# Performance work log

Measured on AMD Instinct MI355X. Metric: run time of the kernel, lower is better.

## Reference

```python
import jax, jax.numpy as jnp
import numpy as np

D_MODEL = 768
HEADS = 12
D_K = D_MODEL // HEADS
NEG = -1e9


def setup_inputs() -> dict:
    key = jax.random.key(0)
    ks = jax.random.split(key, 12)
    B, S = 1, 4096
    q = jax.random.normal(ks[0], (B, S, D_MODEL), dtype=jnp.float32)
    k = jax.random.normal(ks[1], (B, S, D_MODEL), dtype=jnp.float32)
    v = jax.random.normal(ks[2], (B, S, D_MODEL), dtype=jnp.float32)
    mask = jax.random.randint(ks[3], (B, S, S), 0, 2, dtype=jnp.int32)
    sc = 1.0 / np.sqrt(D_MODEL)
    Wq = jax.random.normal(ks[4], (D_MODEL, D_MODEL), dtype=jnp.float32) * sc
    Wk = jax.random.normal(ks[5], (D_MODEL, D_MODEL), dtype=jnp.float32) * sc
    Wv = jax.random.normal(ks[6], (D_MODEL, D_MODEL), dtype=jnp.float32) * sc
    Wo = jax.random.normal(ks[7], (D_MODEL, D_MODEL), dtype=jnp.float32) * sc
    bq = jnp.zeros((D_MODEL,), jnp.float32)
    bk = jnp.zeros((D_MODEL,), jnp.float32)
    bv = jnp.zeros((D_MODEL,), jnp.float32)
    bo = jnp.zeros((D_MODEL,), jnp.float32)
    return {"q": q, "k": k, "v": v, "Wq": Wq, "bq": bq, "Wk": Wk, "bk": bk,
            "Wv": Wv, "bv": bv, "Wo": Wo, "bo": bo, "mask": mask}


def reference(q, k, v, Wq, bq, Wk, bk, Wv, bv, Wo, bo, mask) -> jnp.ndarray:
    B, S, _ = q.shape
    # projections (x @ W^T + b, matching nn.Linear)
    qh = (q @ Wq.T + bq).reshape(B, S, HEADS, D_K).transpose(0, 2, 1, 3)  # [B,h,S,dk]
    kh = (k @ Wk.T + bk).reshape(B, S, HEADS, D_K).transpose(0, 2, 1, 3)
    vh = (v @ Wv.T + bv).reshape(B, S, HEADS, D_K).transpose(0, 2, 1, 3)
    scores = jnp.einsum('bhqd,bhkd->bhqk', qh, kh) / jnp.sqrt(jnp.float32(D_K))
    scores = jnp.where(mask[:, None, :, :] == 0, jnp.float32(NEG), scores)
    attn = jax.nn.softmax(scores, axis=-1)  # dropout disabled (eval mode)
    ctx = jnp.einsum('bhqk,bhkd->bhqd', attn, vh)
    concat = ctx.transpose(0, 2, 1, 3).reshape(B, S, D_MODEL)
    return concat @ Wo.T + bo
```

## Files before the change

### kernel.cpp

```cpp
#include <hip/hip_runtime.h>

#define S_LEN 4096
#define DMODEL 768
#define NHEADS 12
#define DKH 64
#define SC2F 0.18033688011112042f

typedef __attribute__((ext_vector_type(8))) short bf16x8;
typedef __attribute__((ext_vector_type(4))) float f32x4;
typedef __attribute__((ext_vector_type(16))) float f32x16;
typedef __attribute__((ext_vector_type(4))) short s16x4;

#define AS1 __attribute__((address_space(1)))
#define AS3 __attribute__((address_space(3)))

__device__ __forceinline__ short f2bf(float f) {
    union { float f; unsigned u; } x; x.f = f;
    unsigned r = x.u + 0x7fffu + ((x.u >> 16) & 1u);
    return (short)(r >> 16);
}

__device__ __forceinline__ float bf2f(short s) {
    union { unsigned u; float f; } x;
    x.u = ((unsigned)(unsigned short)s) << 16;
    return x.f;
}

__device__ __forceinline__ void gload_lds16(const void* g, void* l) {
    __builtin_amdgcn_global_load_lds((const AS1 void*)g, (AS3 void*)l, 16, 0, 0);
}

__global__ void cvt_all(const float* __restrict__ q, const float* __restrict__ k,
                        const float* __restrict__ v, const float* __restrict__ Wq,
                        const float* __restrict__ Wk, const float* __restrict__ Wv,
                        const float* __restrict__ Wo,
                        short* __restrict__ qb, short* __restrict__ kb,
                        short* __restrict__ vb, short* __restrict__ Wb,
                        const int* __restrict__ mask, unsigned long long* __restrict__ mpT) {
    const int z = blockIdx.z;
    if (z >= 7) {
        int lane = threadIdx.x & 63;
        int wid = (blockIdx.x * blockDim.x + threadIdx.x) >> 6;
        int nw = (gridDim.x * blockDim.x) >> 6;
        int base = (z - 7) * 65536;
        for (int w = base + wid; w < base + 65536; w += nw) {
            int m = mask[(size_t)w * 64 + lane];
            unsigned long long b = __ballot(m != 0);
            if (lane == 0) mpT[(size_t)(w & 63) * S_LEN + (w >> 6)] = b;
        }
        return;
    }
    const float* s;
    short* d;
    int n8;
    if (z < 3) {
        s = z == 0 ? q : z == 1 ? k : v;
        d = z == 0 ? qb : z == 1 ? kb : vb;
        n8 = S_LEN * DMODEL / 8;
    } else {
        s = z == 3 ? Wq : z == 4 ? Wk : z == 5 ? Wv : Wo;
        d = Wb + (size_t)(z - 3) * (DMODEL * DMODEL);
        n8 = DMODEL * DMODEL / 8;
    }
    int stride = gridDim.x * blockDim.x;
    for (int i = blockIdx.x * blockDim.x + threadIdx.x; i < n8; i += stride) {
        float4 x = ((const float4*)s)[2 * i];
        float4 y = ((const float4*)s)[2 * i + 1];
        bf16x8 o;
        o[0] = f2bf(x.x); o[1] = f2bf(x.y); o[2] = f2bf(x.z); o[3] = f2bf(x.w);
        o[4] = f2bf(y.x); o[5] = f2bf(y.y); o[6] = f2bf(y.z); o[7] = f2bf(y.w);
        ((bf16x8*)d)[i] = o;
    }
}

__global__ __launch_bounds__(256) void qkv_gemm(
    const short* __restrict__ qA, const short* __restrict__ kA, const short* __restrict__ vA,
    const short* __restrict__ Wqb, const short* __restrict__ Wkb, const short* __restrict__ Wvb,
    const float* __restrict__ bq, const float* __restrict__ bk, const float* __restrict__ bv,
    short* __restrict__ Qh, short* __restrict__ Kh, short* __restrict__ Vt)
{
    const int z = blockIdx.z;
    const short* A = z == 0 ? qA : z == 1 ? kA : vA;
    const short* B = z == 0 ? Wqb : z == 1 ? Wkb : Wvb;
    const float* bias = z == 0 ? bq : z == 1 ? bk : bv;

    __shared__ __align__(16) short As[128 * 64];
    __shared__ __align__(16) short Bs[128 * 64];
    const int tid = threadIdx.x;
    const int wv = tid >> 6, l = tid & 63;
    const int wr = wv >> 1, wc = wv & 1;
    const int g = l >> 4, hl = l & 15;
    const int m0 = blockIdx.x * 128, n0 = blockIdx.y * 128;
    const int Kd = DMODEL;

    f32x4 acc[4][4] = {};

    for (int kt = 0; kt < Kd; kt += 64) {
        __syncthreads();
        #pragma unroll
        for (int i = 0; i < 4; ++i) {
            int row = i * 32 + wv * 8 + (l >> 3);
            int csrc = (l & 7) ^ (row & 7);
            gload_lds16(A + (size_t)(m0 + row) * Kd + kt + csrc * 8, As + (i * 32 + wv * 8) * 64);
        }
        #pragma unroll
        for (int i = 0; i < 4; ++i) {
            int row = i * 32 + wv * 8 + (l >> 3);
            int csrc = (l & 7) ^ (row & 7);
            gload_lds16(B + (size_t)(n0 + row) * Kd + kt + csrc * 8, Bs + (i * 32 + wv * 8) * 64);
        }
        __syncthreads();
        #pragma unroll
        for (int s = 0; s < 2; ++s) {
            bf16x8 af[4], bf[4];
            #pragma unroll
            for (int m = 0; m < 4; ++m) {
                int row = wr * 64 + m * 16 + hl;
                int ch = (s * 4 + g) ^ (row & 7);
                af[m] = *(const bf16x8*)(As + row * 64 + ch * 8);
            }
            #pragma unroll
            for (int n = 0; n < 4; ++n) {
                int row = wc * 64 + n * 16 + hl;
                int ch = (s * 4 + g) ^ (row & 7);
                bf[n] = *(const bf16x8*)(Bs + row * 64 + ch * 8);
            }
            #pragma unroll
            for (int m = 0; m < 4; ++m)
                #pragma unroll
                for (int n = 0; n < 4; ++n)
                    acc[m][n] = __builtin_amdgcn_mfma_f32_16x16x32_bf16(af[m], bf[n], acc[m][n], 0, 0, 0);
        }
    }

    const float scale = (z == 0) ? SC2F : 1.0f;
    #pragma unroll
    for (int m = 0; m < 4; ++m) {
        #pragma unroll
        for (int n = 0; n < 4; ++n) {
            int gsb = m0 + wr * 64 + m * 16 + g * 4;
            int go = n0 + wc * 64 + n * 16 + hl;
            float bvv = bias[go];
            int hh = go >> 6, d = go & 63;
            if (z == 2) {
                s16x4 p;
                #pragma unroll
                for (int r = 0; r < 4; ++r) p[r] = f2bf(acc[m][n][r] + bvv);
                int gsb2 = (gsb & ~12) | ((gsb & 4) << 1) | ((gsb & 8) >> 1);
                *(s16x4*)(Vt + (size_t)hh * DKH * S_LEN + (size_t)d * S_LEN + gsb2) = p;
            } else {
                short* O = z ? Kh : Qh;
                #pragma unroll
                for (int r = 0; r < 4; ++r)
                    O[(size_t)hh * S_LEN * DKH + (size_t)(gsb + r) * DKH + d] = f2bf((acc[m][n][r] + bvv) * scale);
            }
        }
    }
}

__global__ __launch_bounds__(256) void gemm_out(
    const short* __restrict__ po, const float* __restrict__ pd,
    const short* __restrict__ B,
    const float* __restrict__ bias, float* __restrict__ O)
{
    __shared__ __align__(16) short As[128 * 64];
    __shared__ __align__(16) short Bs[128 * 64];
    const int tid = threadIdx.x;
    const int wv = tid >> 6, l = tid & 63;
    const int wr = wv >> 1, wc = wv & 1;
    const int g = l >> 4, hl = l & 15;
    const int m0 = blockIdx.x * 128, n0 = blockIdx.y * 128;
    const int Kd = DMODEL;

    f32x4 acc[4][4] = {};

    for (int kt = 0; kt < Kd; kt += 64) {
        __syncthreads();
        const int h = kt >> 6;
        #pragma unroll
        for (int i = 0; i < 4; ++i) {
            int row = i * 32 + wv * 8 + (l >> 3);
            int csrc = (l & 7) ^ (row & 7);
            size_t base = ((size_t)h * S_LEN + m0 + row) * DKH + csrc * 8;
            bf16x8 a = *(const bf16x8*)(po + base);
            bf16x8 b = *(const bf16x8*)(po + (size_t)NHEADS * S_LEN * DKH + base);
            float inv = 1.0f / (pd[h * S_LEN + m0 + row] + pd[NHEADS * S_LEN + h * S_LEN + m0 + row]);
            bf16x8 o;
            #pragma unroll
            for (int e = 0; e < 8; ++e)
                o[e] = f2bf((bf2f(a[e]) + bf2f(b[e])) * inv);
            *(bf16x8*)(As + (i * 32 + wv * 8) * 64 + l * 8) = o;
        }
        #pragma unroll
        for (int i = 0; i < 4; ++i) {
            int row = i * 32 + wv * 8 + (l >> 3);
            int csrc = (l & 7) ^ (row & 7);
            gload_lds16(B + (size_t)(n0 + row) * Kd + kt + csrc * 8, Bs + (i * 32 + wv * 8) * 64);
        }
        __syncthreads();
        #pragma unroll
        for (int s = 0; s < 2; ++s) {
            bf16x8 af[4], bf[4];
            #pragma unroll
            for (int m = 0; m < 4; ++m) {
                int row = wr * 64 + m * 16 + hl;
                int ch = (s * 4 + g) ^ (row & 7);
                af[m] = *(const bf16x8*)(As + row * 64 + ch * 8);
            }
            #pragma unroll
            for (int n = 0; n < 4; ++n) {
                int row = wc * 64 + n * 16 + hl;
                int ch = (s * 4 + g) ^ (row & 7);
                bf[n] = *(const bf16x8*)(Bs + row * 64 + ch * 8);
            }
            #pragma unroll
            for (int m = 0; m < 4; ++m)
                #pragma unroll
                for (int n = 0; n < 4; ++n)
                    acc[m][n] = __builtin_amdgcn_mfma_f32_16x16x32_bf16(af[m], bf[n], acc[m][n], 0, 0, 0);
        }
    }

    #pragma unroll
    for (int m = 0; m < 4; ++m) {
        #pragma unroll
        for (int n = 0; n < 4; ++n) {
            int gsb = m0 + wr * 64 + m * 16 + g * 4;
            int go = n0 + wc * 64 + n * 16 + hl;
            float bvv = bias[go];
            #pragma unroll
            for (int r = 0; r < 4; ++r)
                O[(size_t)(gsb + r) * DMODEL + go] = acc[m][n][r] + bvv;
        }
    }
}

__global__ __launch_bounds__(512) void flash_attn6(
    const short* __restrict__ Qh, const short* __restrict__ Kh,
    const short* __restrict__ Vt, const unsigned long long* __restrict__ mpT,
    short* __restrict__ po, float* __restrict__ pd)
{
    __shared__ __align__(16) char pool[35328];

    const int tid = threadIdx.x;
    const int wv = tid >> 6, l = tid & 63;
    const int wq = wv >> 1, sp = wv & 1;
    const int hi = l >> 5, q = l & 31;

    int fid = blockIdx.x;
    int g = (fid & 7) * 96 + (fid >> 3);
    const int h = g >> 6;
    const int sub = g & 63;
    const int half = sub >> 5;
    const int q0 = (sub & 31) * 128;

    const short* Khb = Kh + (size_t)h * S_LEN * DKH;
    const short* Vtb = Vt + (size_t)h * DKH * S_LEN;
    const int qrow = q0 + wq * 32 + q;

    bf16x8 aq[4];
    #pragma unroll
    for (int s = 0; s < 4; ++s)
        aq[s] = *(const bf16x8*)(Qh + (size_t)h * S_LEN * DKH + (size_t)qrow * DKH + s * 16 + hi * 8);

    f32x16 acc[2] = {};
    float dacc[4] = {0.f, 0.f, 0.f, 0.f};

    short* Kl = (short*)(pool + sp * 8192);
    short* Vl = (short*)(pool + 16384 + sp * 8192);

    for (int i = 0; i < 16; ++i) {
        const int kt = half * 32 + i * 2 + sp;
        const int kv0 = kt * 64;
        __syncthreads();
        #pragma unroll
        for (int j = 0; j < 2; ++j) {
            int rp = (wq * 2 + j) * 4 + (l >> 4);
            int x = (l & 15) ^ (rp & 15);
            int row = rp * 2 + (x >> 3);
            int c = x & 7;
            gload_lds16(Khb + (size_t)(kv0 + row) * DKH + c * 8, Kl + (wq * 2 + j) * 512);
            gload_lds16(Vtb + (size_t)row * S_LEN + kv0 + c * 8, Vl + (wq * 2 + j) * 512);
        }
        unsigned long long w = mpT[(size_t)kt * S_LEN + qrow];
        __syncthreads();

        unsigned long long w2 = w >> (hi * 4);
        unsigned mlo = (unsigned)w2, mhi2 = (unsigned)(w2 >> 32);

        #pragma unroll
        for (int t = 0; t < 2; ++t) {
            const unsigned msk = t ? mhi2 : mlo;
            f32x16 st = {};
            __builtin_amdgcn_s_setprio(1);
            #pragma unroll
            for (int s = 0; s < 4; ++s) {
                int rowb = t * 32 + q;
                int rp = rowb >> 1;
                int ch = (((rowb & 1) << 3) + (s * 2 + hi)) ^ (rp & 15);
                bf16x8 kf = *(const bf16x8*)(Kl + rp * 128 + ch * 8);
                st = __builtin_amdgcn_mfma_f32_32x32x16_bf16(kf, aq[s], st, 0, 0, 0);
            }
            __builtin_amdgcn_s_setprio(0);
            float pf[16];
            #pragma unroll
            for (int r = 0; r < 16; ++r) {
                const int cbit = (r & 3) + 8 * (r >> 2);
                float sv = (msk & (1u << cbit)) ? st[r] : -120.0f;
                pf[r] = __builtin_amdgcn_exp2f(sv);
                dacc[r & 3] += pf[r];
            }
            __builtin_amdgcn_s_setprio(1);
            #pragma unroll
            for (int kk = 0; kk < 2; ++kk) {
                const float* pp = pf + kk * 8;
                union { unsigned u[4]; bf16x8 v; } pa;
                asm("v_cvt_pk_bf16_f32 %0, %1, %2" : "=v"(pa.u[0]) : "v"(pp[0]), "v"(pp[1]));
                asm("v_cvt_pk_bf16_f32 %0, %1, %2" : "=v"(pa.u[1]) : "v"(pp[2]), "v"(pp[3]));
                asm("v_cvt_pk_bf16_f32 %0, %1, %2" : "=v"(pa.u[2]) : "v"(pp[4]), "v"(pp[5]));
                asm("v_cvt_pk_bf16_f32 %0, %1, %2" : "=v"(pa.u[3]) : "v"(pp[6]), "v"(pp[7]));
                const int ks = t * 2 + kk;
                #pragma unroll
                for (int dt = 0; dt < 2; ++dt) {
                    int rowb = dt * 32 + q;
                    int rp = rowb >> 1;
                    int ch = (((rowb & 1) << 3) + (ks * 2 + hi)) ^ (rp & 15);
                    bf16x8 vf = *(const bf16x8*)(Vl + rp * 128 + ch * 8);
                    acc[dt] = __builtin_amdgcn_mfma_f32_32x32x16_bf16(pa.v, vf, acc[dt], 0, 0, 0);
                }
            }
            __builtin_amdgcn_s_setprio(0);
        }
    }

    const float dsum = dacc[0] + dacc[1] + dacc[2] + dacc[3];

    __syncthreads();
    float* accb = (float*)pool;
    float* ddb  = (float*)(pool + 32768);
    ddb[wv * 64 + l] = dsum;
    if (sp == 1) {
        #pragma unroll
        for (int dt = 0; dt < 2; ++dt)
            #pragma unroll
            for (int r = 0; r < 16; ++r)
                accb[(((wq * 2 + dt) * 16 + r) << 6) + l] = acc[dt][r];
    }
    __syncthreads();
    if (sp == 0) {
        float dq = ddb[(wq * 2) * 64 + q] + ddb[(wq * 2) * 64 + 32 + q]
                 + ddb[(wq * 2 + 1) * 64 + q] + ddb[(wq * 2 + 1) * 64 + 32 + q];
        if (hi == 0) pd[(size_t)half * (NHEADS * S_LEN) + (size_t)h * S_LEN + q0 + wq * 32 + q] = dq;
        #pragma unroll
        for (int dt = 0; dt < 2; ++dt) {
            #pragma unroll
            for (int r = 0; r < 16; ++r) {
                float o = acc[dt][r] + accb[(((wq * 2 + dt) * 16 + r) << 6) + l];
                int qo = (r & 3) + 8 * (r >> 2) + 4 * hi;
                po[((size_t)(half * NHEADS + h) * S_LEN + q0 + wq * 32 + qo) * DKH + dt * 32 + q] = f2bf(o);
            }
        }
    }
}

extern "C" void kernel_launch(void* const* d_in, const int* in_sizes, int n_in,
                              void* d_out, int out_size, void* d_ws, size_t ws_size,
                              hipStream_t stream) {
    (void)in_sizes; (void)n_in; (void)out_size; (void)ws_size;
    const float* q  = (const float*)d_in[0];
    const float* k  = (const float*)d_in[1];
    const float* v  = (const float*)d_in[2];
    const float* Wq = (const float*)d_in[3];
    const float* bq = (const float*)d_in[4];
    const float* Wk = (const float*)d_in[5];
    const float* bk = (const float*)d_in[6];
    const float* Wv = (const float*)d_in[7];
    const float* bv = (const float*)d_in[8];
    const float* Wo = (const float*)d_in[9];
    const float* bo = (const float*)d_in[10];
    const int* mask = (const int*)d_in[11];

    char* ws = (char*)d_ws;
    short* qb  = (short*)(ws + 0);
    short* kb  = (short*)(ws + 6291456);
    short* vb  = (short*)(ws + 12582912);
    short* Wqb = (short*)(ws + 18874368);
    short* Wkb = (short*)(ws + 20054016);
    short* Wvb = (short*)(ws + 21233664);
    short* Wob = (short*)(ws + 22413312);
    short* Qh  = (short*)(ws + 23592960);
    short* Kh  = (short*)(ws + 29884416);
    short* Vt  = (short*)(ws + 36175872);
    unsigned long long* mpT = (unsigned long long*)(ws + 42467328);
    short* po = (short*)(ws + 0);
    float* pd = (float*)(ws + 12582912);

    cvt_all<<<dim3(512, 1, 11), 256, 0, stream>>>(q, k, v, Wq, Wk, Wv, Wo, qb, kb, vb, Wqb, mask, mpT);

    qkv_gemm<<<dim3(S_LEN / 128, DMODEL / 128, 3), 256, 0, stream>>>(
        qb, kb, vb, Wqb, Wkb, Wvb, bq, bk, bv, Qh, Kh, Vt);

    flash_attn6<<<768, 512, 0, stream>>>(Qh, Kh, Vt, mpT, po, pd);

    gemm_out<<<dim3(S_LEN / 128, DMODEL / 128), 256, 0, stream>>>(po, pd, Wob, bo, (float*)d_out);
}
```

Baseline: 164.3 us.

## Fuse fp32-to-bf16 activation conversion and mask packing into QKV GEMM

Drops the separate pass that converted q/k/v to bf16 in workspace. The QKV GEMM now loads fp32 activations directly, converts them in registers with packed bf16 conversion instructions, and stores them into swizzled LDS. Mask bit-packing moves into extra z-slices of the GEMM launch, with 4 ballots unrolled per loop iteration, and a small kernel still converts the weights. This saves a full write and re-read of the bf16 activations, but the A tile loses its async global-to-LDS load and the GEMM blocks now share the GPU with mask-packing blocks.

```diff
diff --git a/kernel.cpp b/kernel.cpp
--- a/kernel.cpp
+++ b/kernel.cpp
@@ -30,57 +30,55 @@
     __builtin_amdgcn_global_load_lds((const AS1 void*)g, (AS3 void*)l, 16, 0, 0);
 }
 
-__global__ void cvt_all(const float* __restrict__ q, const float* __restrict__ k,
-                        const float* __restrict__ v, const float* __restrict__ Wq,
-                        const float* __restrict__ Wk, const float* __restrict__ Wv,
-                        const float* __restrict__ Wo,
-                        short* __restrict__ qb, short* __restrict__ kb,
-                        short* __restrict__ vb, short* __restrict__ Wb,
-                        const int* __restrict__ mask, unsigned long long* __restrict__ mpT) {
-    const int z = blockIdx.z;
-    if (z >= 7) {
-        int lane = threadIdx.x & 63;
-        int wid = (blockIdx.x * blockDim.x + threadIdx.x) >> 6;
-        int nw = (gridDim.x * blockDim.x) >> 6;
-        int base = (z - 7) * 65536;
-        for (int w = base + wid; w < base + 65536; w += nw) {
-            int m = mask[(size_t)w * 64 + lane];
-            unsigned long long b = __ballot(m != 0);
-            if (lane == 0) mpT[(size_t)(w & 63) * S_LEN + (w >> 6)] = b;
-        }
-        return;
-    }
-    const float* s;
-    short* d;
-    int n8;
-    if (z < 3) {
-        s = z == 0 ? q : z == 1 ? k : v;
-        d = z == 0 ? qb : z == 1 ? kb : vb;
-        n8 = S_LEN * DMODEL / 8;
-    } else {
-        s = z == 3 ? Wq : z == 4 ? Wk : z == 5 ? Wv : Wo;
-        d = Wb + (size_t)(z - 3) * (DMODEL * DMODEL);
-        n8 = DMODEL * DMODEL / 8;
-    }
-    int stride = gridDim.x * blockDim.x;
-    for (int i = blockIdx.x * blockDim.x + threadIdx.x; i < n8; i += stride) {
-        float4 x = ((const float4*)s)[2 * i];
-        float4 y = ((const float4*)s)[2 * i + 1];
-        bf16x8 o;
-        o[0] = f2bf(x.x); o[1] = f2bf(x.y); o[2] = f2bf(x.z); o[3] = f2bf(x.w);
-        o[4] = f2bf(y.x); o[5] = f2bf(y.y); o[6] = f2bf(y.z); o[7] = f2bf(y.w);
-        ((bf16x8*)d)[i] = o;
-    }
+__global__ void cvt_w(const float* __restrict__ Wq, const float* __restrict__ Wk,
+                      const float* __restrict__ Wv, const float* __restrict__ Wo,
+                      short* __restrict__ Wb) {
+    const float* s = blockIdx.z == 0 ? Wq : blockIdx.z == 1 ? Wk : blockIdx.z == 2 ? Wv : Wo;
+    short* d = Wb + (size_t)blockIdx.z * (DMODEL * DMODEL);
+    int i = blockIdx.x * blockDim.x + threadIdx.x;
+    float4 x = ((const float4*)s)[2 * i];
+    float4 y = ((const float4*)s)[2 * i + 1];
+    bf16x8 o;
+    o[0] = f2bf(x.x); o[1] = f2bf(x.y); o[2] = f2bf(x.z); o[3] = f2bf(x.w);
+    o[4] = f2bf(y.x); o[5] = f2bf(y.y); o[6] = f2bf(y.z); o[7] = f2bf(y.w);
+    ((bf16x8*)d)[i] = o;
 }
 
 __global__ __launch_bounds__(256) void qkv_gemm(
-    const short* __restrict__ qA, const short* __restrict__ kA, const short* __restrict__ vA,
+    const float* __restrict__ qA, const float* __restrict__ kA, const float* __restrict__ vA,
     const short* __restrict__ Wqb, const short* __restrict__ Wkb, const short* __restrict__ Wvb,
     const float* __restrict__ bq, const float* __restrict__ bk, const float* __restrict__ bv,
-    short* __restrict__ Qh, short* __restrict__ Kh, short* __restrict__ Vt)
+    short* __restrict__ Qh, short* __restrict__ Kh, short* __restrict__ Vt,
+    const int* __restrict__ mask, unsigned long long* __restrict__ mpT)
 {
     const int z = blockIdx.z;
-    const short* A = z == 0 ? qA : z == 1 ? kA : vA;
+    if (z >= 3) {
+        const int TOT = S_LEN * S_LEN / 64;
+        const int NW = 1536;
+        int lane = threadIdx.x & 63;
+        int bid = blockIdx.x + blockIdx.y * gridDim.x + (z - 3) * 192;
+        int wid = ((bid << 8) + threadIdx.x) >> 6;
+        for (int w = wid; w < TOT; w += 4 * NW) {
+            int w1 = w + NW, w2 = w + 2 * NW, w3 = w + 3 * NW;
+            int a = mask[(size_t)w * 64 + lane];
+            int b = (w1 < TOT) ? mask[(size_t)w1 * 64 + lane] : 0;
+            int c = (w2 < TOT) ? mask[(size_t)w2 * 64 + lane] : 0;
+            int d = (w3 < TOT) ? mask[(size_t)w3 * 64 + lane] : 0;
+            unsigned long long b0 = __ballot(a != 0);
+            unsigned long long b1 = __ballot(b != 0);
+            unsigned long long b2 = __ballot(c != 0);
+            unsigned long long b3 = __ballot(d != 0);
+            if (lane == 0) {
+                mpT[(size_t)(w & 63) * S_LEN + (w >> 6)] = b0;
+                if (w1 < TOT) mpT[(size_t)(w1 & 63) * S_LEN + (w1 >> 6)] = b1;
+                if (w2 < TOT) mpT[(size_t)(w2 & 63) * S_LEN + (w2 >> 6)] = b2;
+                if (w3 < TOT) mpT[(size_t)(w3 & 63) * S_LEN + (w3 >> 6)] = b3;
+            }
+        }
+        return;
+    }
+
+    const float* A32 = z == 0 ? qA : z == 1 ? kA : vA;
     const short* B = z == 0 ? Wqb : z == 1 ? Wkb : Wvb;
     const float* bias = z == 0 ? bq : z == 1 ? bk : bv;
 
@@ -100,8 +98,17 @@
         #pragma unroll
         for (int i = 0; i < 4; ++i) {
             int row = i * 32 + wv * 8 + (l >> 3);
-            int csrc = (l & 7) ^ (row & 7);
-            gload_lds16(A + (size_t)(m0 + row) * Kd + kt + csrc * 8, As + (i * 32 + wv * 8) * 64);
+            int c = l & 7;
+            int gc = c ^ (row & 7);
+            const float* src = A32 + (size_t)(m0 + row) * Kd + kt + gc * 8;
+            float4 x = *(const float4*)(src);
+            float4 y = *(const float4*)(src + 4);
+            union { unsigned u[4]; bf16x8 v; } o;
+            asm("v_cvt_pk_bf16_f32 %0, %1, %2" : "=v"(o.u[0]) : "v"(x.x), "v"(x.y));
+            asm("v_cvt_pk_bf16_f32 %0, %1, %2" : "=v"(o.u[1]) : "v"(x.z), "v"(x.w));
+            asm("v_cvt_pk_bf16_f32 %0, %1, %2" : "=v"(o.u[2]) : "v"(y.x), "v"(y.y));
+            asm("v_cvt_pk_bf16_f32 %0, %1, %2" : "=v"(o.u[3]) : "v"(y.z), "v"(y.w));
+            *(bf16x8*)(As + row * 64 + c * 8) = o.v;
         }
         #pragma unroll
         for (int i = 0; i < 4; ++i) {
@@ -381,9 +388,6 @@
     const int* mask = (const int*)d_in[11];
 
     char* ws = (char*)d_ws;
-    short* qb  = (short*)(ws + 0);
-    short* kb  = (short*)(ws + 6291456);
-    short* vb  = (short*)(ws + 12582912);
     short* Wqb = (short*)(ws + 18874368);
     short* Wkb = (short*)(ws + 20054016);
     short* Wvb = (short*)(ws + 21233664);
@@ -395,10 +399,10 @@
     short* po = (short*)(ws + 0);
     float* pd = (float*)(ws + 12582912);
 
-    cvt_all<<<dim3(512, 1, 11), 256, 0, stream>>>(q, k, v, Wq, Wk, Wv, Wo, qb, kb, vb, Wqb, mask, mpT);
-
-    qkv_gemm<<<dim3(S_LEN / 128, DMODEL / 128, 3), 256, 0, stream>>>(
-        qb, kb, vb, Wqb, Wkb, Wvb, bq, bk, bv, Qh, Kh, Vt);
+    cvt_w<<<dim3(288, 1, 4), 256, 0, stream>>>(Wq, Wk, Wv, Wo, Wqb);
+
+    qkv_gemm<<<dim3(S_LEN / 128, DMODEL / 128, 5), 256, 0, stream>>>(
+        q, k, v, Wqb, Wkb, Wvb, bq, bk, bv, Qh, Kh, Vt, mask, mpT);
 
     flash_attn6<<<768, 512, 0, stream>>>(Qh, Kh, Vt, mpT, po, pd);
 
```

Measured after the change: 179.3 us. 9.1% more time.
